# Kernel tuning notes

Hardware: AMD Instinct MI355X
Metric: run time of the kernel (lower is better)

## Reference

```python
import jax, jax.numpy as jnp
import numpy as np

B, T, S, U = 64, 64, 128, 4  # batch, frames, yt_img_size, upscale_factor
P, U2 = S * S, U * U          # per-pixel batch dim, tiny-matmul output dim
RECON = S * U                 # 512


def setup_inputs() -> dict:
    key = jax.random.key(0)
    k1, k2, k3 = jax.random.split(key, 3)
    yt = jax.random.normal(k1, (B, T, S, S), dtype=jnp.float32)
    weights = jax.random.normal(k2, (P, T, U2), dtype=jnp.float32)
    biases = jax.random.normal(k3, (P, 1, U2), dtype=jnp.float32)
    return {"yt": yt, "weights": weights, "biases": biases}


def reference(yt, weights, biases):
    # (B, T, S, S) -> (P, B, T): one tiny (B,T)x(T,U2) GEMM per pixel location
    y = yt.reshape(B, T, P).transpose(2, 0, 1)
    # per-location batched matmul + bias: (P, B, U2)
    up = jnp.einsum('pbt,ptu->pbu', y, weights) + biases
    # pixel-shuffle style upsampling: (S, S, B, U, U) -> (B, S, U, S, U) -> (B, 1, 512, 512)
    up = up.reshape(S, S, B, U, U).transpose(2, 0, 3, 1, 4)
    out = up.reshape(B, RECON, RECON)[:, None, :, :]
    # seq_block is identity in this configuration
    return out
```

## Files before the change

### kernel.cpp

```cpp
#include <hip/hip_runtime.h>

namespace {
constexpr int Sdim = 128;
constexpr int Tdim = 64;
constexpr int U2c  = 16;
constexpr int PT   = 32;
constexpr int NTHREADS = 512;
constexpr int PP = Sdim * Sdim;
constexpr int TQ = 16;
constexpr int NSTG = Tdim / TQ;
}

__global__ __launch_bounds__(NTHREADS, 2)
void upscale_fused(const float* __restrict__ yt,
                   const float* __restrict__ wgt,
                   const float* __restrict__ bias,
                   float* __restrict__ out)
{
    __shared__ float wlds[TQ * U2c * PT];

    const int tid   = threadIdx.x;
    const int p_blk = blockIdx.x * PT;

    const int pg = tid & 15;
    const int b2 = (tid >> 4) & 31;
    const int p0 = p_blk + pg * 2;

    auto stage = [&](int stg) {
        const float4* wgt4 = reinterpret_cast<const float4*>(wgt);
        #pragma unroll
        for (int i = 0; i < 4; ++i) {
            const int f  = i * NTHREADS + tid;
            const int r  = f >> 6;
            const int c  = f & 63;
            const int tw = c >> 2;
            const int uq = c & 3;
            const float4 v = wgt4[(size_t)(p_blk + r) * 256 + (size_t)stg * 64 + c];
            const int col = r ^ (2 * tw);
            float* dst = &wlds[(tw * U2c + uq * 4) * PT + col];
            dst[0 * PT] = v.x;  dst[1 * PT] = v.y;  dst[2 * PT] = v.z;  dst[3 * PT] = v.w;
        }
    };

    stage(0);

    float acc[2][2][16];
    #pragma unroll
    for (int jp = 0; jp < 2; ++jp) {
        const float* bp = bias + (size_t)(p0 + jp) * U2c;
        const float4 q0 = *reinterpret_cast<const float4*>(bp + 0);
        const float4 q1 = *reinterpret_cast<const float4*>(bp + 4);
        const float4 q2 = *reinterpret_cast<const float4*>(bp + 8);
        const float4 q3 = *reinterpret_cast<const float4*>(bp + 12);
        const float bb[16] = {q0.x,q0.y,q0.z,q0.w, q1.x,q1.y,q1.z,q1.w,
                              q2.x,q2.y,q2.z,q2.w, q3.x,q3.y,q3.z,q3.w};
        #pragma unroll
        for (int u = 0; u < 16; ++u) { acc[0][jp][u] = bb[u]; acc[1][jp][u] = bb[u]; }
    }

    const float* y0b = yt + (size_t)b2 * ((size_t)Tdim * PP) + p0;
    const float* y1b = y0b + (size_t)32 * Tdim * PP;
    auto ldy = [&](int t, float2& a, float2& b) {
        a = *reinterpret_cast<const float2*>(y0b + (size_t)t * PP);
        b = *reinterpret_cast<const float2*>(y1b + (size_t)t * PP);
    };

    auto step = [&](const float2& ya, const float2& yb, int tl) {
        const float* wrow = &wlds[tl * (U2c * PT) + ((pg * 2) ^ (2 * tl))];
        #pragma unroll
        for (int u = 0; u < 16; ++u) {
            const float2 wv = *reinterpret_cast<const float2*>(wrow + u * PT);
            acc[0][0][u] = fmaf(ya.x, wv.x, acc[0][0][u]);
            acc[0][1][u] = fmaf(ya.y, wv.y, acc[0][1][u]);
            acc[1][0][u] = fmaf(yb.x, wv.x, acc[1][0][u]);
            acc[1][1][u] = fmaf(yb.y, wv.y, acc[1][1][u]);
        }
    };

    float2 A0, A1, B0, B1, C0, C1, D0, D1;
    ldy(0, A0, A1); ldy(1, B0, B1); ldy(2, C0, C1); ldy(3, D0, D1);

    __syncthreads();

    #pragma unroll 1
    for (int stg = 0; stg < NSTG; ++stg) {
        if (stg) {
            __syncthreads();
            stage(stg);
            __syncthreads();
        }
        #pragma unroll 1
        for (int tq = 0; tq < TQ; tq += 4) {
            const int tg = stg * TQ + tq;
            step(A0, A1, tq + 0); { const int tf = (tg + 4 < Tdim) ? tg + 4 : Tdim - 1; ldy(tf, A0, A1); }
            step(B0, B1, tq + 1); { const int tf = (tg + 5 < Tdim) ? tg + 5 : Tdim - 1; ldy(tf, B0, B1); }
            step(C0, C1, tq + 2); { const int tf = (tg + 6 < Tdim) ? tg + 6 : Tdim - 1; ldy(tf, C0, C1); }
            step(D0, D1, tq + 3); { const int tf = (tg + 7 < Tdim) ? tg + 7 : Tdim - 1; ldy(tf, D0, D1); }
        }
    }

    const int s1   = p_blk / Sdim;
    const int s2_0 = p_blk % Sdim;

    #pragma unroll
    for (int bi = 0; bi < 2; ++bi) {
        const int b = b2 + bi * 32;
        float* ob = out + (size_t)b * (512 * 512);
        #pragma unroll
        for (int jp = 0; jp < 2; ++jp) {
            const int c0 = (s2_0 + pg * 2 + jp) * 4;
            #pragma unroll
            for (int u1 = 0; u1 < 4; ++u1) {
                const int r = s1 * 4 + u1;
                float4 v;
                v.x = acc[bi][jp][u1 * 4 + 0];
                v.y = acc[bi][jp][u1 * 4 + 1];
                v.z = acc[bi][jp][u1 * 4 + 2];
                v.w = acc[bi][jp][u1 * 4 + 3];
                *reinterpret_cast<float4*>(ob + (size_t)r * 512 + c0) = v;
            }
        }
    }
}

extern "C" void kernel_launch(void* const* d_in, const int* in_sizes, int n_in,
                              void* d_out, int out_size, void* d_ws, size_t ws_size,
                              hipStream_t stream)
{
    const float* yt   = (const float*)d_in[0];
    const float* wgt  = (const float*)d_in[1];
    const float* bias = (const float*)d_in[2];
    float* outp       = (float*)d_out;

    dim3 grid(PP / PT);
    dim3 block(NTHREADS);
    hipLaunchKernelGGL(upscale_fused, grid, block, 0, stream, yt, wgt, bias, outp);
}
```

Before: 103.9 us.

## Drop LDS weight staging; split U2 across thread halves and read weights from global

Removes the shared-memory weight tile and its per-stage barriers. Each thread now handles 4 batches, 2 pixels and half of the 16 outputs, and loads weights straight from global memory as float4s (which should mostly hit L1/L2, since the 16 batch-group threads share them). This raises y reuse per weight and removes LDS traffic and synchronisation. In exchange it issues redundant global weight loads and uses a shorter y prefetch depth.

```diff
diff --git a/kernel.cpp b/kernel.cpp
--- a/kernel.cpp
+++ b/kernel.cpp
@@ -7,8 +7,6 @@
 constexpr int PT   = 32;
 constexpr int NTHREADS = 512;
 constexpr int PP = Sdim * Sdim;
-constexpr int TQ = 16;
-constexpr int NSTG = Tdim / TQ;
 }
 
 __global__ __launch_bounds__(NTHREADS, 2)
@@ -17,106 +15,95 @@
                    const float* __restrict__ bias,
                    float* __restrict__ out)
 {
-    __shared__ float wlds[TQ * U2c * PT];
-
     const int tid   = threadIdx.x;
     const int p_blk = blockIdx.x * PT;
 
     const int pg = tid & 15;
-    const int b2 = (tid >> 4) & 31;
+    const int bq = (tid >> 4) & 15;
+    const int ug = tid >> 8;
     const int p0 = p_blk + pg * 2;
 
-    auto stage = [&](int stg) {
-        const float4* wgt4 = reinterpret_cast<const float4*>(wgt);
+    const float4* wgt4 = reinterpret_cast<const float4*>(wgt);
+    const float4* wr0  = wgt4 + (size_t)p0 * 256 + 2 * ug;
+    const float4* wr1  = wr0 + 256;
+
+    float acc[4][2][8];
+    #pragma unroll
+    for (int jp = 0; jp < 2; ++jp) {
+        const float* bp = bias + (size_t)(p0 + jp) * U2c + ug * 8;
+        const float4 q0 = *reinterpret_cast<const float4*>(bp);
+        const float4 q1 = *reinterpret_cast<const float4*>(bp + 4);
+        const float bb[8] = {q0.x,q0.y,q0.z,q0.w, q1.x,q1.y,q1.z,q1.w};
         #pragma unroll
-        for (int i = 0; i < 4; ++i) {
-            const int f  = i * NTHREADS + tid;
-            const int r  = f >> 6;
-            const int c  = f & 63;
-            const int tw = c >> 2;
-            const int uq = c & 3;
-            const float4 v = wgt4[(size_t)(p_blk + r) * 256 + (size_t)stg * 64 + c];
-            const int col = r ^ (2 * tw);
-            float* dst = &wlds[(tw * U2c + uq * 4) * PT + col];
-            dst[0 * PT] = v.x;  dst[1 * PT] = v.y;  dst[2 * PT] = v.z;  dst[3 * PT] = v.w;
+        for (int k = 0; k < 4; ++k)
+            #pragma unroll
+            for (int j = 0; j < 8; ++j) acc[k][jp][j] = bb[j];
+    }
+
+    const float* ybase = yt + (size_t)bq * ((size_t)Tdim * PP) + p0;
+    auto ldy = [&](int t, float2* dst) {
+        #pragma unroll
+        for (int k = 0; k < 4; ++k)
+            dst[k] = *reinterpret_cast<const float2*>(
+                ybase + (size_t)k * 16 * Tdim * PP + (size_t)t * PP);
+    };
+
+    auto step = [&](int t, const float2* y) {
+        const float4 wa0 = wr0[t * 4];
+        const float4 wa1 = wr0[t * 4 + 1];
+        const float4 wb0 = wr1[t * 4];
+        const float4 wb1 = wr1[t * 4 + 1];
+        #pragma unroll
+        for (int k = 0; k < 4; ++k) {
+            acc[k][0][0] = fmaf(y[k].x, wa0.x, acc[k][0][0]);
+            acc[k][0][1] = fmaf(y[k].x, wa0.y, acc[k][0][1]);
+            acc[k][0][2] = fmaf(y[k].x, wa0.z, acc[k][0][2]);
+            acc[k][0][3] = fmaf(y[k].x, wa0.w, acc[k][0][3]);
+            acc[k][0][4] = fmaf(y[k].x, wa1.x, acc[k][0][4]);
+            acc[k][0][5] = fmaf(y[k].x, wa1.y, acc[k][0][5]);
+            acc[k][0][6] = fmaf(y[k].x, wa1.z, acc[k][0][6]);
+            acc[k][0][7] = fmaf(y[k].x, wa1.w, acc[k][0][7]);
+            acc[k][1][0] = fmaf(y[k].y, wb0.x, acc[k][1][0]);
+            acc[k][1][1] = fmaf(y[k].y, wb0.y, acc[k][1][1]);
+            acc[k][1][2] = fmaf(y[k].y, wb0.z, acc[k][1][2]);
+            acc[k][1][3] = fmaf(y[k].y, wb0.w, acc[k][1][3]);
+            acc[k][1][4] = fmaf(y[k].y, wb1.x, acc[k][1][4]);
+            acc[k][1][5] = fmaf(y[k].y, wb1.y, acc[k][1][5]);
+            acc[k][1][6] = fmaf(y[k].y, wb1.z, acc[k][1][6]);
+            acc[k][1][7] = fmaf(y[k].y, wb1.w, acc[k][1][7]);
         }
     };
 
-    stage(0);
-
-    float acc[2][2][16];
-    #pragma unroll
-    for (int jp = 0; jp < 2; ++jp) {
-        const float* bp = bias + (size_t)(p0 + jp) * U2c;
-        const float4 q0 = *reinterpret_cast<const float4*>(bp + 0);
-        const float4 q1 = *reinterpret_cast<const float4*>(bp + 4);
-        const float4 q2 = *reinterpret_cast<const float4*>(bp + 8);
-        const float4 q3 = *reinterpret_cast<const float4*>(bp + 12);
-        const float bb[16] = {q0.x,q0.y,q0.z,q0.w, q1.x,q1.y,q1.z,q1.w,
-                              q2.x,q2.y,q2.z,q2.w, q3.x,q3.y,q3.z,q3.w};
-        #pragma unroll
-        for (int u = 0; u < 16; ++u) { acc[0][jp][u] = bb[u]; acc[1][jp][u] = bb[u]; }
-    }
-
-    const float* y0b = yt + (size_t)b2 * ((size_t)Tdim * PP) + p0;
-    const float* y1b = y0b + (size_t)32 * Tdim * PP;
-    auto ldy = [&](int t, float2& a, float2& b) {
-        a = *reinterpret_cast<const float2*>(y0b + (size_t)t * PP);
-        b = *reinterpret_cast<const float2*>(y1b + (size_t)t * PP);
-    };
-
-    auto step = [&](const float2& ya, const float2& yb, int tl) {
-        const float* wrow = &wlds[tl * (U2c * PT) + ((pg * 2) ^ (2 * tl))];
-        #pragma unroll
-        for (int u = 0; u < 16; ++u) {
-            const float2 wv = *reinterpret_cast<const float2*>(wrow + u * PT);
-            acc[0][0][u] = fmaf(ya.x, wv.x, acc[0][0][u]);
-            acc[0][1][u] = fmaf(ya.y, wv.y, acc[0][1][u]);
-            acc[1][0][u] = fmaf(yb.x, wv.x, acc[1][0][u]);
-            acc[1][1][u] = fmaf(yb.y, wv.y, acc[1][1][u]);
-        }
-    };
-
-    float2 A0, A1, B0, B1, C0, C1, D0, D1;
-    ldy(0, A0, A1); ldy(1, B0, B1); ldy(2, C0, C1); ldy(3, D0, D1);
-
-    __syncthreads();
+    float2 yc[4], yn[4];
+    ldy(0, yc);
+    ldy(1, yn);
 
     #pragma unroll 1
-    for (int stg = 0; stg < NSTG; ++stg) {
-        if (stg) {
-            __syncthreads();
-            stage(stg);
-            __syncthreads();
-        }
-        #pragma unroll 1
-        for (int tq = 0; tq < TQ; tq += 4) {
-            const int tg = stg * TQ + tq;
-            step(A0, A1, tq + 0); { const int tf = (tg + 4 < Tdim) ? tg + 4 : Tdim - 1; ldy(tf, A0, A1); }
-            step(B0, B1, tq + 1); { const int tf = (tg + 5 < Tdim) ? tg + 5 : Tdim - 1; ldy(tf, B0, B1); }
-            step(C0, C1, tq + 2); { const int tf = (tg + 6 < Tdim) ? tg + 6 : Tdim - 1; ldy(tf, C0, C1); }
-            step(D0, D1, tq + 3); { const int tf = (tg + 7 < Tdim) ? tg + 7 : Tdim - 1; ldy(tf, D0, D1); }
-        }
+    for (int t = 0; t < Tdim; t += 2) {
+        step(t, yc);
+        if (t + 2 < Tdim) ldy(t + 2, yc);
+        step(t + 1, yn);
+        if (t + 3 < Tdim) ldy(t + 3, yn);
     }
 
     const int s1   = p_blk / Sdim;
     const int s2_0 = p_blk % Sdim;
 
     #pragma unroll
-    for (int bi = 0; bi < 2; ++bi) {
-        const int b = b2 + bi * 32;
+    for (int k = 0; k < 4; ++k) {
+        const int b = bq + 16 * k;
         float* ob = out + (size_t)b * (512 * 512);
         #pragma unroll
         for (int jp = 0; jp < 2; ++jp) {
             const int c0 = (s2_0 + pg * 2 + jp) * 4;
             #pragma unroll
-            for (int u1 = 0; u1 < 4; ++u1) {
-                const int r = s1 * 4 + u1;
+            for (int half = 0; half < 2; ++half) {
+                const int r = s1 * 4 + ug * 2 + half;
                 float4 v;
-                v.x = acc[bi][jp][u1 * 4 + 0];
-                v.y = acc[bi][jp][u1 * 4 + 1];
-                v.z = acc[bi][jp][u1 * 4 + 2];
-                v.w = acc[bi][jp][u1 * 4 + 3];
+                v.x = acc[k][jp][half * 4 + 0];
+                v.y = acc[k][jp][half * 4 + 1];
+                v.z = acc[k][jp][half * 4 + 2];
+                v.w = acc[k][jp][half * 4 + 3];
                 *reinterpret_cast<float4*>(ob + (size_t)r * 512 + c0) = v;
             }
         }
```

Result: slower. 186.5 us (+79.4%).

## Split U2 outputs across two thread halves with 1024-thread blocks

Applied to the files above, without the earlier changes.

Doubles the block to 1024 threads and splits the 16 upscale outputs between two thread groups, so each thread keeps 32 accumulators instead of 64. This cuts register pressure and raises occupancy to hide latency. The cost is that every y value is now loaded by two threads, doubling global yt reads (likely served from L1/L2). The y prefetch depth also drops from 4 timesteps to 2, and the weight stage load is split across more threads.

```diff
diff --git a/kernel.cpp b/kernel.cpp
--- a/kernel.cpp
+++ b/kernel.cpp
@@ -5,13 +5,13 @@
 constexpr int Tdim = 64;
 constexpr int U2c  = 16;
 constexpr int PT   = 32;
-constexpr int NTHREADS = 512;
+constexpr int NTHREADS = 1024;
 constexpr int PP = Sdim * Sdim;
 constexpr int TQ = 16;
 constexpr int NSTG = Tdim / TQ;
 }
 
-__global__ __launch_bounds__(NTHREADS, 2)
+__global__ __launch_bounds__(NTHREADS, 8)
 void upscale_fused(const float* __restrict__ yt,
                    const float* __restrict__ wgt,
                    const float* __restrict__ bias,
@@ -24,51 +24,52 @@
 
     const int pg = tid & 15;
     const int b2 = (tid >> 4) & 31;
+    const int ug = tid >> 9;
     const int p0 = p_blk + pg * 2;
 
+    const float4* wgt4 = reinterpret_cast<const float4*>(wgt);
+
     auto stage = [&](int stg) {
-        const float4* wgt4 = reinterpret_cast<const float4*>(wgt);
         #pragma unroll
-        for (int i = 0; i < 4; ++i) {
-            const int f  = i * NTHREADS + tid;
-            const int r  = f >> 6;
-            const int c  = f & 63;
+        for (int i = 0; i < 2; ++i) {
+            const int f = i * NTHREADS + tid;
+            const int r = f >> 6;
+            const int c = f & 63;
+            const float4 v = wgt4[(size_t)(p_blk + r) * 256 + (size_t)stg * 64 + c];
             const int tw = c >> 2;
             const int uq = c & 3;
-            const float4 v = wgt4[(size_t)(p_blk + r) * 256 + (size_t)stg * 64 + c];
             const int col = r ^ (2 * tw);
             float* dst = &wlds[(tw * U2c + uq * 4) * PT + col];
-            dst[0 * PT] = v.x;  dst[1 * PT] = v.y;  dst[2 * PT] = v.z;  dst[3 * PT] = v.w;
+            dst[0 * PT] = v.x;  dst[1 * PT] = v.y;
+            dst[2 * PT] = v.z;  dst[3 * PT] = v.w;
         }
     };
 
     stage(0);
 
-    float acc[2][2][16];
+    float acc[2][2][8];
     #pragma unroll
     for (int jp = 0; jp < 2; ++jp) {
-        const float* bp = bias + (size_t)(p0 + jp) * U2c;
-        const float4 q0 = *reinterpret_cast<const float4*>(bp + 0);
+        const float* bp = bias + (size_t)(p0 + jp) * U2c + ug * 8;
+        const float4 q0 = *reinterpret_cast<const float4*>(bp);
         const float4 q1 = *reinterpret_cast<const float4*>(bp + 4);
-        const float4 q2 = *reinterpret_cast<const float4*>(bp + 8);
-        const float4 q3 = *reinterpret_cast<const float4*>(bp + 12);
-        const float bb[16] = {q0.x,q0.y,q0.z,q0.w, q1.x,q1.y,q1.z,q1.w,
-                              q2.x,q2.y,q2.z,q2.w, q3.x,q3.y,q3.z,q3.w};
+        const float bb[8] = {q0.x,q0.y,q0.z,q0.w, q1.x,q1.y,q1.z,q1.w};
         #pragma unroll
-        for (int u = 0; u < 16; ++u) { acc[0][jp][u] = bb[u]; acc[1][jp][u] = bb[u]; }
+        for (int j = 0; j < 8; ++j) { acc[0][jp][j] = bb[j]; acc[1][jp][j] = bb[j]; }
     }
 
     const float* y0b = yt + (size_t)b2 * ((size_t)Tdim * PP) + p0;
     const float* y1b = y0b + (size_t)32 * Tdim * PP;
-    auto ldy = [&](int t, float2& a, float2& b) {
-        a = *reinterpret_cast<const float2*>(y0b + (size_t)t * PP);
-        b = *reinterpret_cast<const float2*>(y1b + (size_t)t * PP);
-    };
+    float2 yc0, yc1, yn0, yn1;
+    yc0 = *reinterpret_cast<const float2*>(y0b);
+    yc1 = *reinterpret_cast<const float2*>(y1b);
+    yn0 = *reinterpret_cast<const float2*>(y0b + PP);
+    yn1 = *reinterpret_cast<const float2*>(y1b + PP);
 
     auto step = [&](const float2& ya, const float2& yb, int tl) {
-        const float* wrow = &wlds[tl * (U2c * PT) + ((pg * 2) ^ (2 * tl))];
+        const float* wrow = &wlds[((pg * 2) ^ (2 * tl)) + tl * (U2c * PT) + (ug * 8) * PT];
         #pragma unroll
-        for (int u = 0; u < 16; ++u) {
+        for (int u = 0; u < 8; ++u) {
             const float2 wv = *reinterpret_cast<const float2*>(wrow + u * PT);
             acc[0][0][u] = fmaf(ya.x, wv.x, acc[0][0][u]);
             acc[0][1][u] = fmaf(ya.y, wv.y, acc[0][1][u]);
@@ -77,25 +78,28 @@
         }
     };
 
-    float2 A0, A1, B0, B1, C0, C1, D0, D1;
-    ldy(0, A0, A1); ldy(1, B0, B1); ldy(2, C0, C1); ldy(3, D0, D1);
-
     __syncthreads();
 
     #pragma unroll 1
     for (int stg = 0; stg < NSTG; ++stg) {
-        if (stg) {
+        #pragma unroll 1
+        for (int tq = 0; tq < TQ; tq += 2) {
+            const int tg = stg * TQ + tq;
+            step(yc0, yc1, tq);
+            if (tg + 2 < Tdim) {
+                yc0 = *reinterpret_cast<const float2*>(y0b + (size_t)(tg + 2) * PP);
+                yc1 = *reinterpret_cast<const float2*>(y1b + (size_t)(tg + 2) * PP);
+            }
+            step(yn0, yn1, tq + 1);
+            if (tg + 3 < Tdim) {
+                yn0 = *reinterpret_cast<const float2*>(y0b + (size_t)(tg + 3) * PP);
+                yn1 = *reinterpret_cast<const float2*>(y1b + (size_t)(tg + 3) * PP);
+            }
+        }
+        if (stg + 1 < NSTG) {
             __syncthreads();
-            stage(stg);
+            stage(stg + 1);
             __syncthreads();
-        }
-        #pragma unroll 1
-        for (int tq = 0; tq < TQ; tq += 4) {
-            const int tg = stg * TQ + tq;
-            step(A0, A1, tq + 0); { const int tf = (tg + 4 < Tdim) ? tg + 4 : Tdim - 1; ldy(tf, A0, A1); }
-            step(B0, B1, tq + 1); { const int tf = (tg + 5 < Tdim) ? tg + 5 : Tdim - 1; ldy(tf, B0, B1); }
-            step(C0, C1, tq + 2); { const int tf = (tg + 6 < Tdim) ? tg + 6 : Tdim - 1; ldy(tf, C0, C1); }
-            step(D0, D1, tq + 3); { const int tf = (tg + 7 < Tdim) ? tg + 7 : Tdim - 1; ldy(tf, D0, D1); }
         }
     }
 
@@ -110,13 +114,13 @@
         for (int jp = 0; jp < 2; ++jp) {
             const int c0 = (s2_0 + pg * 2 + jp) * 4;
             #pragma unroll
-            for (int u1 = 0; u1 < 4; ++u1) {
-                const int r = s1 * 4 + u1;
+            for (int half = 0; half < 2; ++half) {
+                const int r = s1 * 4 + ug * 2 + half;
                 float4 v;
-                v.x = acc[bi][jp][u1 * 4 + 0];
-                v.y = acc[bi][jp][u1 * 4 + 1];
-                v.z = acc[bi][jp][u1 * 4 + 2];
-                v.w = acc[bi][jp][u1 * 4 + 3];
+                v.x = acc[bi][jp][half * 4 + 0];
+                v.y = acc[bi][jp][half * 4 + 1];
+                v.z = acc[bi][jp][half * 4 + 2];
+                v.w = acc[bi][jp][half * 4 + 3];
                 *reinterpret_cast<float4*>(ob + (size_t)r * 512 + c0) = v;
             }
         }
```

After: 198.9 us. +91.3%, slower.
